# Kernel tuning notes

Hardware: AMD Instinct MI355X
Metric: run time of the kernel (lower is better)

## Reference

```python
import jax, jax.numpy as jnp
import numpy as np

C0 = 16          # embed channels (c0) == mamba d_model
OUT_DIM = 32
D_INNER = 32     # expand * c0
D_STATE = 16
D_CONV = 4
DT_RANK = 1      # max(1, d_model // 16)
EPS = 1e-5


def setup_inputs():
    key = jax.random.key(0)
    ks = jax.random.split(key, 32)

    def n(i, shape, s):
        return (jax.random.normal(ks[i], shape) * s).astype(jnp.float32)

    inp = {
        "x": jax.random.normal(ks[0], (1, 4, 64, 64, 64), jnp.float32),
        "embed_w": n(1, (4, C0, 1, 7, 7, 7), 0.1),   # 4 per-modality conv7 stems
        "ln_g": jnp.ones((C0,), jnp.float32),
        "ln_b": jnp.zeros((C0,), jnp.float32),
        "in_proj_w": n(2, (2 * D_INNER, C0), 0.25),
        "out_proj_w": n(3, (C0, D_INNER), 0.18),
        "up_w": n(4, (C0, OUT_DIM, 2, 2, 2), 0.2),   # ConvTranspose3d k=2 s=2
    }
    for j, sfx in enumerate(["", "_b"]):             # forward / backward scan params
        b = 5 + 7 * j
        inp["conv_w" + sfx] = n(b, (D_INNER, 1, D_CONV), 0.3)
        inp["conv_b" + sfx] = n(b + 1, (D_INNER,), 0.1)
        inp["xproj_w" + sfx] = n(b + 2, (DT_RANK + 2 * D_STATE, D_INNER), 0.15)
        inp["dtproj_w" + sfx] = n(b + 3, (D_INNER, DT_RANK), 0.5)
        inp["dtproj_b" + sfx] = jnp.full((D_INNER,), -4.6, jnp.float32)  # softplus ~= 0.01
        inp["A_log" + sfx] = jnp.log(jnp.tile(jnp.arange(1, D_STATE + 1, dtype=jnp.float32), (D_INNER, 1)))
        inp["D_skip" + sfx] = jnp.ones((D_INNER,), jnp.float32)
    return inp


def _instnorm(x):
    m = jnp.mean(x, axis=(2, 3, 4), keepdims=True)
    v = jnp.mean(jnp.square(x - m), axis=(2, 3, 4), keepdims=True)
    return (x - m) / jnp.sqrt(v + EPS)


def _embed(x1, w):
    # Conv3d(1, c0, k=7, s=2, p=3, bias=False) -> InstanceNorm3d -> GELU(exact)
    y = jax.lax.conv_general_dilated(x1, w, (2, 2, 2), [(3, 3)] * 3,
                                     dimension_numbers=('NCDHW', 'OIDHW', 'NCDHW'))
    return jax.nn.gelu(_instnorm(y), approximate=False)


def _branch(u, z, cw, cb, xw, dtw, dtb, A_log, D_skip):
    # One Mamba scan branch. u, z: [B, L, Dn]
    Dn = u.shape[-1]
    uc = jax.lax.conv_general_dilated(jnp.swapaxes(u, 1, 2), cw, (1,), [(D_CONV - 1, 0)],
                                      feature_group_count=Dn,
                                      dimension_numbers=('NCH', 'OIH', 'NCH'))
    u = jax.nn.silu(jnp.swapaxes(uc + cb[None, :, None], 1, 2))       # causal dw-conv + SiLU
    xdbl = u @ xw.T                                                   # [B,L,R+2N]
    dt = jax.nn.softplus(xdbl[..., :DT_RANK] @ dtw.T + dtb)           # [B,L,Dn]
    Bm = xdbl[..., DT_RANK:DT_RANK + D_STATE]                         # [B,L,N]
    Cm = xdbl[..., DT_RANK + D_STATE:]                                # [B,L,N]
    A = -jnp.exp(A_log)                                               # [Dn,N]
    a = jnp.exp(dt[..., None] * A)                                    # [B,L,Dn,N]
    b = (dt * u)[..., None] * Bm[:, :, None, :]                       # [B,L,Dn,N]

    def comb(c1, c2):
        a1, b1 = c1
        a2, b2 = c2
        return a1 * a2, a2 * b1 + b2

    _, h = jax.lax.associative_scan(comb, (a, b), axis=1)             # h_t = a_t h_{t-1} + b_t
    y = jnp.einsum('bldn,bln->bld', h, Cm) + u * D_skip
    return y * jax.nn.silu(z)


def _bimamba(t, p):
    xz = t @ p['in_proj_w'].T
    xi, z = jnp.split(xz, 2, axis=-1)
    yf = _branch(xi, z, p['conv_w'], p['conv_b'], p['xproj_w'], p['dtproj_w'],
                 p['dtproj_b'], p['A_log'], p['D_skip'])
    yb = _branch(xi[:, ::-1], z[:, ::-1], p['conv_w_b'], p['conv_b_b'], p['xproj_w_b'],
                 p['dtproj_w_b'], p['dtproj_b_b'], p['A_log_b'], p['D_skip_b'])[:, ::-1]
    return (yf + yb) @ p['out_proj_w'].T


def _mamba_dir(x5, p):
    B, C = x5.shape[:2]
    t = jnp.swapaxes(x5.reshape(B, C, -1), 1, 2)                      # [B, L, C]
    mu = jnp.mean(t, axis=-1, keepdims=True)
    var = jnp.mean(jnp.square(t - mu), axis=-1, keepdims=True)
    t = (t - mu) / jnp.sqrt(var + EPS) * p['ln_g'] + p['ln_b']        # LayerNorm
    t = _bimamba(t, p)
    return jnp.swapaxes(t, 1, 2).reshape(x5.shape)


def _mamba_layer(x5, p):
    # tri-directional scans: (d,w,h), (w,d,h), (h,w,d) + residual
    o1 = _mamba_dir(x5, p)
    o2 = jnp.transpose(_mamba_dir(jnp.transpose(x5, (0, 1, 3, 2, 4)), p), (0, 1, 3, 2, 4))
    o3 = jnp.transpose(_mamba_dir(jnp.transpose(x5, (0, 1, 4, 3, 2)), p), (0, 1, 4, 3, 2))
    return o1 + o2 + o3 + x5


def reference(x, embed_w, ln_g, ln_b, in_proj_w, out_proj_w, up_w,
              conv_w, conv_b, xproj_w, dtproj_w, dtproj_b, A_log, D_skip,
              conv_w_b, conv_b_b, xproj_w_b, dtproj_w_b, dtproj_b_b, A_log_b, D_skip_b):
    p = dict(ln_g=ln_g, ln_b=ln_b, in_proj_w=in_proj_w, out_proj_w=out_proj_w,
             conv_w=conv_w, conv_b=conv_b, xproj_w=xproj_w, dtproj_w=dtproj_w,
             dtproj_b=dtproj_b, A_log=A_log, D_skip=D_skip,
             conv_w_b=conv_w_b, conv_b_b=conv_b_b, xproj_w_b=xproj_w_b,
             dtproj_w_b=dtproj_w_b, dtproj_b_b=dtproj_b_b, A_log_b=A_log_b,
             D_skip_b=D_skip_b)
    us = [_embed(x[:, m:m + 1], embed_w[m]) for m in range(4)]        # 4 modalities
    outs = [_mamba_layer(u, p) for u in us]
    y = outs[0] + outs[1] + outs[2] + outs[3] + us[0] + us[1] + us[2] + us[3]
    B, _, D, H, W = y.shape
    # ConvTranspose3d(c0, out_dim, k=2, s=2): each output 2x2x2 block from one input voxel
    y = jnp.einsum('bcdhw,coijk->bodihjwk', y, up_w).reshape(B, OUT_DIM, 2 * D, 2 * H, 2 * W)
    return y
```

## Files before the change

kernel.cpp:

```cpp
#include <hip/hip_runtime.h>
#include <math.h>

#define L 32768
#define CH 64
#define NC 512

__device__ __forceinline__ int sigma_map(int l, int perm) {
    int b2 = l >> 10, b1 = (l >> 5) & 31, b0 = l & 31;
    if (perm == 0) return (b2 << 10) | (b1 << 5) | b0;
    if (perm == 1) return (b1 << 10) | (b2 << 5) | b0;
    return (b0 << 10) | (b1 << 5) | b2;
}

__device__ __forceinline__ float silu_f(float v) {
    return v / (1.f + __expf(-v));
}
__device__ __forceinline__ float softplus_f(float x) {
    return fmaxf(x, 0.f) + log1pf(__expf(-fabsf(x)));
}

__device__ __forceinline__ float row16_sum(float x) {
    int v;
    v = __builtin_amdgcn_update_dpp(0, __float_as_int(x), 0x128, 0xf, 0xf, true);
    x += __int_as_float(v);
    v = __builtin_amdgcn_update_dpp(0, __float_as_int(x), 0x124, 0xf, 0xf, true);
    x += __int_as_float(v);
    v = __builtin_amdgcn_update_dpp(0, __float_as_int(x), 0x122, 0xf, 0xf, true);
    x += __int_as_float(v);
    v = __builtin_amdgcn_update_dpp(0, __float_as_int(x), 0x121, 0xf, 0xf, true);
    x += __int_as_float(v);
    return x;
}

__global__ __launch_bounds__(256) void k_embed(const float* __restrict__ x,
                                               const float* __restrict__ w,
                                               float* __restrict__ us) {
    __shared__ float tile[10143];
    int bx = blockIdx.x, m = blockIdx.y;
    int c = bx >> 7, sb = bx & 127;
    int zc = sb >> 2, yc0 = (sb & 3) << 3;
    const float* xin = x + m * 262144;
    int iz0 = 2 * zc - 3, iy0 = 2 * yc0 - 3;
    for (int i = threadIdx.x; i < 10143; i += 256) {
        int tz = i / 1449, r = i - tz * 1449;
        int ty = r / 69, tx = r - ty * 69;
        int gz = iz0 + tz, gy = iy0 + ty, gx = tx - 3;
        float v = 0.f;
        if ((unsigned)gz < 64u && (unsigned)gy < 64u && (unsigned)gx < 64u)
            v = xin[(gz * 64 + gy) * 64 + gx];
        tile[i] = v;
    }
    __syncthreads();
    const float* wc = w + (m * 16 + c) * 343;
    int tyl = threadIdx.x >> 5, xc = threadIdx.x & 31;
    float acc = 0.f;
    for (int kz = 0; kz < 7; ++kz)
        for (int ky = 0; ky < 7; ++ky) {
            const float* row = &tile[(kz * 21 + 2 * tyl + ky) * 69 + 2 * xc];
            const float* wr = &wc[kz * 49 + ky * 7];
            #pragma unroll
            for (int kx = 0; kx < 7; ++kx) acc += row[kx] * wr[kx];
        }
    us[(m * 16 + c) * 32768 + sb * 256 + threadIdx.x] = acc;
}

__global__ void k_instnorm_gelu(float* __restrict__ us) {
    int ch = blockIdx.x;
    float* p = us + ch * 32768;
    float s = 0.f, s2 = 0.f;
    for (int i = threadIdx.x; i < 32768; i += 256) { float v = p[i]; s += v; s2 += v * v; }
    __shared__ float rs[256], rs2[256];
    rs[threadIdx.x] = s; rs2[threadIdx.x] = s2;
    __syncthreads();
    for (int o = 128; o > 0; o >>= 1) {
        if (threadIdx.x < o) { rs[threadIdx.x] += rs[threadIdx.x + o]; rs2[threadIdx.x] += rs2[threadIdx.x + o]; }
        __syncthreads();
    }
    float mu = rs[0] * (1.f / 32768.f);
    float var = rs2[0] * (1.f / 32768.f) - mu * mu;
    float rinv = rsqrtf(var + 1e-5f);
    for (int i = threadIdx.x; i < 32768; i += 256) {
        float v = (p[i] - mu) * rinv;
        p[i] = 0.5f * v * (1.f + erff(v * 0.70710678118654752f));
    }
}

__global__ void k_transpose(const float* __restrict__ us, float* __restrict__ us_t) {
    __shared__ float tl[16][257];
    int m = blockIdx.x >> 7, t0 = (blockIdx.x & 127) << 8;
    for (int i = threadIdx.x; i < 4096; i += 256) {
        int c = i >> 8, j = i & 255;
        tl[c][j] = us[(m * 16 + c) * 32768 + t0 + j];
    }
    __syncthreads();
    for (int i = threadIdx.x; i < 4096; i += 256) {
        int j = i >> 4, c = i & 15;
        us_t[(m * 32768 + t0 + j) * 16 + c] = tl[c][j];
    }
}

__global__ __launch_bounds__(512) void k_chunkA(
    const float* __restrict__ us_t, const float* __restrict__ ln_g, const float* __restrict__ ln_b,
    const float* __restrict__ Wip,
    const float* __restrict__ cwA, const float* __restrict__ cbA, const float* __restrict__ xwA,
    const float* __restrict__ dtwA, const float* __restrict__ dtbA, const float* __restrict__ AlA,
    const float* __restrict__ cwB, const float* __restrict__ cbB, const float* __restrict__ xwB,
    const float* __restrict__ dtwB, const float* __restrict__ dtbB, const float* __restrict__ AlB,
    float2* __restrict__ hlPa) {
    __shared__ float sm[7808];
    float* xiT = sm;
    float* uSh = sm + 2304;
    float* sB  = sm + 4480;
    float* xd0 = sm + 5568;
    float* G   = sm + 5632;

    int c = blockIdx.x, dir = blockIdx.y;
    int m = dir / 3, perm = dir - m * 3;
    int p0 = c * CH;
    int tid = threadIdx.x;

    G[tid] = Wip[tid];
    if (tid < 16) G[512 + tid] = ln_g[tid];
    else if (tid < 32) G[512 + tid] = ln_b[tid - 16];
    __syncthreads();

    if (tid < 70) {
        int p = p0 - 3 + tid;
        if ((unsigned)p < (unsigned)L) {
            int sp = sigma_map(p, perm);
            const float4* rw = (const float4*)(us_t + (m * 32768 + sp) * 16);
            float t[16];
            ((float4*)t)[0] = rw[0]; ((float4*)t)[1] = rw[1];
            ((float4*)t)[2] = rw[2]; ((float4*)t)[3] = rw[3];
            float mu = 0.f;
            #pragma unroll
            for (int ci = 0; ci < 16; ++ci) mu += t[ci];
            mu *= (1.f / 16.f);
            float var = 0.f;
            #pragma unroll
            for (int ci = 0; ci < 16; ++ci) { float d = t[ci] - mu; var += d * d; }
            var *= (1.f / 16.f);
            float rinv = rsqrtf(var + 1e-5f);
            #pragma unroll
            for (int ci = 0; ci < 16; ++ci)
                uSh[ci * 72 + tid] = (t[ci] - mu) * rinv * G[512 + ci] + G[528 + ci];
        } else {
            #pragma unroll
            for (int ci = 0; ci < 16; ++ci) uSh[ci * 72 + tid] = 0.f;
        }
    }
    __syncthreads();

    for (int it = tid; it < 576; it += 512) {
        int d = it / 18, q = it - d * 18;
        float ax = 0.f, ay = 0.f, az = 0.f, aw = 0.f;
        #pragma unroll
        for (int ci = 0; ci < 16; ++ci) {
            float4 tq = *(const float4*)&uSh[ci * 72 + 4 * q];
            float wv = G[d * 16 + ci];
            ax += tq.x * wv; ay += tq.y * wv; az += tq.z * wv; aw += tq.w * wv;
        }
        float4 o4 = {ax, ay, az, aw};
        *(float4*)&xiT[d * 72 + 4 * q] = o4;
    }
    __syncthreads();

    for (int b = 0; b < 2; ++b) {
        const float* cw  = b ? cwB  : cwA;
        const float* cb  = b ? cbB  : cbA;
        const float* xw  = b ? xwB  : xwA;
        const float* dtw = b ? dtwB : dtwA;
        const float* dtb = b ? dtbB : dtbA;
        const float* Al  = b ? AlB  : AlA;
        for (int i = tid; i < 544; i += 512) G[i] = xw[i];
        if (tid < 128) G[544 + tid] = cw[tid];
        else if (tid < 160) G[544 + tid] = cb[tid - 128];
        __syncthreads();

        {
            int d = tid >> 4, q = tid & 15, s0 = 4 * q;
            float xr[7];
            if (b == 0) {
                #pragma unroll
                for (int j = 0; j < 7; ++j) xr[j] = xiT[d * 72 + s0 + j];
            } else {
                #pragma unroll
                for (int j = 0; j < 7; ++j) xr[j] = xiT[d * 72 + 63 - s0 + j];
            }
            float w0 = G[544 + d * 4], w1 = G[545 + d * 4], w2 = G[546 + d * 4], w3 = G[547 + d * 4];
            float bias = G[672 + d];
            #pragma unroll
            for (int i = 0; i < 4; ++i) {
                float a;
                if (b == 0) a = bias + xr[i] * w0 + xr[i + 1] * w1 + xr[i + 2] * w2 + xr[i + 3] * w3;
                else        a = bias + xr[6 - i] * w0 + xr[5 - i] * w1 + xr[4 - i] * w2 + xr[3 - i] * w3;
                uSh[d * 68 + s0 + i] = silu_f(a);
            }
        }
        __syncthreads();

        for (int it = tid; it < 272; it += 512) {
            int j = it >> 4, q = it & 15, s0 = 4 * q;
            float ax = 0.f, ay = 0.f, az = 0.f, aw = 0.f;
            #pragma unroll
            for (int ci = 0; ci < 32; ++ci) {
                float4 uq = *(const float4*)&uSh[ci * 68 + s0];
                float wv = G[j * 32 + ci];
                ax += uq.x * wv; ay += uq.y * wv; az += uq.z * wv; aw += uq.w * wv;
            }
            float4 o4 = {ax, ay, az, aw};
            if (j == 0) *(float4*)&xd0[s0] = o4;
            else        *(float4*)&sB[(j - 1) * 68 + s0] = o4;
        }
        __syncthreads();

        for (int i = tid; i < 2048; i += 512) {
            int d2 = i >> 6, s = i & 63;
            G[d2 * 68 + s] = softplus_f(xd0[s] * dtw[d2] + dtb[d2]);
        }
        __syncthreads();

        {
            int d = tid >> 4, n = tid & 15;
            float A = -__expf(Al[tid]);
            float h = 0.f, sumdt = 0.f;
            const float* dtp = &G[d * 68];
            const float* up  = &uSh[d * 68];
            const float* Bp  = &sB[n * 68];
            for (int s0 = 0; s0 < CH; s0 += 4) {
                float4 dt4 = *(const float4*)&dtp[s0];
                float4 u4  = *(const float4*)&up[s0];
                float4 B4  = *(const float4*)&Bp[s0];
                h = fmaf(__expf(dt4.x * A), h, dt4.x * u4.x * B4.x);
                h = fmaf(__expf(dt4.y * A), h, dt4.y * u4.y * B4.y);
                h = fmaf(__expf(dt4.z * A), h, dt4.z * u4.z * B4.z);
                h = fmaf(__expf(dt4.w * A), h, dt4.w * u4.w * B4.w);
                sumdt += (dt4.x + dt4.y) + (dt4.z + dt4.w);
            }
            int chunk = b ? (NC - 1 - c) : c;
            float2 v; v.x = h; v.y = __expf(sumdt * A);
            hlPa[(((size_t)(dir * 2 + b) * NC + chunk) * 512) + tid] = v;
        }
        __syncthreads();
    }
}

__global__ __launch_bounds__(512) void k_scanB(float2* __restrict__ hlPa) {
    int db = blockIdx.x;
    int t = threadIdx.x;
    float2* base = hlPa + (size_t)db * NC * 512 + t;
    float H = 0.f;
    for (int c0 = 0; c0 < NC; c0 += 8) {
        float2 v[8];
        #pragma unroll
        for (int j = 0; j < 8; ++j) v[j] = base[(c0 + j) * 512];
        #pragma unroll
        for (int j = 0; j < 8; ++j) {
            *((float*)(base + (c0 + j) * 512)) = H;
            H = fmaf(v[j].y, H, v[j].x);
        }
    }
}

__global__ __launch_bounds__(512) void k_chunkC(
    const float* __restrict__ us_t, const float* __restrict__ ln_g, const float* __restrict__ ln_b,
    const float* __restrict__ Wip, const float* __restrict__ Wout,
    const float* __restrict__ cwA, const float* __restrict__ cbA, const float* __restrict__ xwA,
    const float* __restrict__ dtwA, const float* __restrict__ dtbA, const float* __restrict__ AlA,
    const float* __restrict__ DsA,
    const float* __restrict__ cwB, const float* __restrict__ cbB, const float* __restrict__ xwB,
    const float* __restrict__ dtwB, const float* __restrict__ dtbB, const float* __restrict__ AlB,
    const float* __restrict__ DsB,
    const float2* __restrict__ hlPa, float* __restrict__ O) {
    __shared__ float sm[13376];
    float* xiT = sm;
    float* zT  = sm + 2304;
    float* syT = sm + 4608;
    float* uSh = sm + 6784;
    float* sB  = sm + 8960;
    float* sC  = sm + 10048;
    float* xd0 = sm + 11136;
    float* G   = sm + 11200;

    int c = blockIdx.x, dir = blockIdx.y;
    int m = dir / 3, perm = dir - m * 3;
    int p0 = c * CH;
    int tid = threadIdx.x;

    for (int i = tid; i < 1024; i += 512) G[i] = Wip[i];
    if (tid < 16) G[1024 + tid] = ln_g[tid];
    else if (tid < 32) G[1024 + tid] = ln_b[tid - 16];
    __syncthreads();

    if (tid < 70) {
        int p = p0 - 3 + tid;
        if ((unsigned)p < (unsigned)L) {
            int sp = sigma_map(p, perm);
            const float4* rw = (const float4*)(us_t + (m * 32768 + sp) * 16);
            float t[16];
            ((float4*)t)[0] = rw[0]; ((float4*)t)[1] = rw[1];
            ((float4*)t)[2] = rw[2]; ((float4*)t)[3] = rw[3];
            float mu = 0.f;
            #pragma unroll
            for (int ci = 0; ci < 16; ++ci) mu += t[ci];
            mu *= (1.f / 16.f);
            float var = 0.f;
            #pragma unroll
            for (int ci = 0; ci < 16; ++ci) { float d = t[ci] - mu; var += d * d; }
            var *= (1.f / 16.f);
            float rinv = rsqrtf(var + 1e-5f);
            #pragma unroll
            for (int ci = 0; ci < 16; ++ci)
                uSh[ci * 72 + tid] = (t[ci] - mu) * rinv * G[1024 + ci] + G[1040 + ci];
        } else {
            #pragma unroll
            for (int ci = 0; ci < 16; ++ci) uSh[ci * 72 + tid] = 0.f;
        }
    }
    __syncthreads();

    for (int it = tid; it < 1152; it += 512) {
        int dd = it / 18, q = it - dd * 18;
        float ax = 0.f, ay = 0.f, az = 0.f, aw = 0.f;
        #pragma unroll
        for (int ci = 0; ci < 16; ++ci) {
            float4 tq = *(const float4*)&uSh[ci * 72 + 4 * q];
            float wv = G[dd * 16 + ci];
            ax += tq.x * wv; ay += tq.y * wv; az += tq.z * wv; aw += tq.w * wv;
        }
        float4 o4 = {ax, ay, az, aw};
        int d = dd & 31;
        if (dd < 32) *(float4*)&xiT[d * 72 + 4 * q] = o4;
        else         *(float4*)&zT[d * 72 + 4 * q] = o4;
    }
    __syncthreads();

    for (int b = 0; b < 2; ++b) {
        const float* cw  = b ? cwB  : cwA;
        const float* cb  = b ? cbB  : cbA;
        const float* xw  = b ? xwB  : xwA;
        const float* dtw = b ? dtwB : dtwA;
        const float* dtb = b ? dtbB : dtbA;
        const float* Al  = b ? AlB  : AlA;
        const float* Ds  = b ? DsB  : DsA;
        for (int i = tid; i < 1056; i += 512) G[i] = xw[i];
        if (tid < 128) G[1056 + tid] = cw[tid];
        else if (tid < 160) G[1056 + tid] = cb[tid - 128];
        __syncthreads();

        {
            int d = tid >> 4, q = tid & 15, s0 = 4 * q;
            float xr[7];
            if (b == 0) {
                #pragma unroll
                for (int j = 0; j < 7; ++j) xr[j] = xiT[d * 72 + s0 + j];
            } else {
                #pragma unroll
                for (int j = 0; j < 7; ++j) xr[j] = xiT[d * 72 + 63 - s0 + j];
            }
            float w0 = G[1056 + d * 4], w1 = G[1057 + d * 4], w2 = G[1058 + d * 4], w3 = G[1059 + d * 4];
            float bias = G[1184 + d];
            #pragma unroll
            for (int i = 0; i < 4; ++i) {
                float a;
                if (b == 0) a = bias + xr[i] * w0 + xr[i + 1] * w1 + xr[i + 2] * w2 + xr[i + 3] * w3;
                else        a = bias + xr[6 - i] * w0 + xr[5 - i] * w1 + xr[4 - i] * w2 + xr[3 - i] * w3;
                uSh[d * 68 + s0 + i] = silu_f(a);
            }
        }
        __syncthreads();

        for (int it = tid; it < 528; it += 512) {
            int j = it >> 4, q = it & 15, s0 = 4 * q;
            float ax = 0.f, ay = 0.f, az = 0.f, aw = 0.f;
            #pragma unroll
            for (int ci = 0; ci < 32; ++ci) {
                float4 uq = *(const float4*)&uSh[ci * 68 + s0];
                float wv = G[j * 32 + ci];
                ax += uq.x * wv; ay += uq.y * wv; az += uq.z * wv; aw += uq.w * wv;
            }
            float4 o4 = {ax, ay, az, aw};
            if (j == 0)      *(float4*)&xd0[s0] = o4;
            else if (j < 17) *(float4*)&sB[(j - 1) * 68 + s0] = o4;
            else             *(float4*)&sC[(j - 17) * 68 + s0] = o4;
        }
        __syncthreads();

        for (int i = tid; i < 2048; i += 512) {
            int d2 = i >> 6, s = i & 63;
            G[d2 * 68 + s] = softplus_f(xd0[s] * dtw[d2] + dtb[d2]);
        }
        __syncthreads();

        {
            int d = tid >> 4, n = tid & 15;
            float A = -__expf(Al[tid]);
            int chunk = b ? (NC - 1 - c) : c;
            float h = hlPa[(((size_t)(dir * 2 + b) * NC + chunk) * 512) + tid].x;
            const float* dtp = &G[d * 68];
            const float* up  = &uSh[d * 68];
            const float* Bp  = &sB[n * 68];
            const float* Cp  = &sC[n * 68];
            for (int s0 = 0; s0 < CH; s0 += 4) {
                float4 dt4 = *(const float4*)&dtp[s0];
                float4 u4  = *(const float4*)&up[s0];
                float4 B4  = *(const float4*)&Bp[s0];
                float4 C4  = *(const float4*)&Cp[s0];
                float pr0, pr1, pr2, pr3;
                h = fmaf(__expf(dt4.x * A), h, dt4.x * u4.x * B4.x); pr0 = row16_sum(h * C4.x);
                h = fmaf(__expf(dt4.y * A), h, dt4.y * u4.y * B4.y); pr1 = row16_sum(h * C4.y);
                h = fmaf(__expf(dt4.z * A), h, dt4.z * u4.z * B4.z); pr2 = row16_sum(h * C4.z);
                h = fmaf(__expf(dt4.w * A), h, dt4.w * u4.w * B4.w); pr3 = row16_sum(h * C4.w);
                if (n == 0) {
                    if (b == 0) {
                        float4 o4 = {pr0, pr1, pr2, pr3};
                        *(float4*)&syT[d * 68 + s0] = o4;
                    } else {
                        float4* dst = (float4*)&syT[d * 68 + (60 - s0)];
                        float4 old = *dst;
                        old.x += pr3; old.y += pr2; old.z += pr1; old.w += pr0;
                        *dst = old;
                    }
                }
            }
        }
        __syncthreads();

        for (int it = tid; it < 2048; it += 512) {
            int d = it >> 6, s = it & 63;
            int pl = b ? (63 - s) : s;
            syT[d * 68 + pl] += uSh[d * 68 + s] * Ds[d];
        }
        __syncthreads();
    }

    for (int it = tid; it < 2048; it += 512) {
        int d = it >> 6, pl = it & 63;
        syT[d * 68 + pl] *= silu_f(zT[d * 72 + pl + 3]);
    }
    __syncthreads();

    if (tid < 512) G[tid] = Wout[tid];
    __syncthreads();
    for (int it = tid; it < 1024; it += 512) {
        int p = it >> 4, cc = it & 15;
        float acc = 0.f;
        #pragma unroll
        for (int d = 0; d < 32; ++d) acc += syT[d * 68 + p] * G[cc * 32 + d];
        O[((size_t)(dir * 32768 + p0 + p)) * 16 + cc] = acc;
    }
}

__global__ void k_accum(const float* __restrict__ us_t, const float* __restrict__ O,
                        float* __restrict__ acc_t) {
    int it = blockIdx.x * 256 + threadIdx.x;
    int sp = it >> 2, q = (it & 3) << 2;
    float ax = 0.f, ay = 0.f, az = 0.f, aw = 0.f;
    #pragma unroll
    for (int mm = 0; mm < 4; ++mm) {
        float4 v = *(const float4*)&us_t[(mm * 32768 + sp) * 16 + q];
        ax += 2.f * v.x; ay += 2.f * v.y; az += 2.f * v.z; aw += 2.f * v.w;
    }
    #pragma unroll
    for (int perm = 0; perm < 3; ++perm) {
        int l = sigma_map(sp, perm);
        #pragma unroll
        for (int mm = 0; mm < 4; ++mm) {
            int dir = mm * 3 + perm;
            float4 v = *(const float4*)&O[(dir * 32768 + l) * 16 + q];
            ax += v.x; ay += v.y; az += v.z; aw += v.w;
        }
    }
    float4 o4 = {ax, ay, az, aw};
    *(float4*)&acc_t[sp * 16 + q] = o4;
}

__global__ void k_up(const float* __restrict__ acc_t, const float* __restrict__ upw,
                     float* __restrict__ out) {
    __shared__ float w[4096];
    for (int i = threadIdx.x; i < 4096; i += 256) w[i] = upw[i];
    __syncthreads();
    int e = blockIdx.x * 256 + threadIdx.x;
    int o = e >> 17;
    int r2 = e & 131071;
    int Dz = r2 >> 11, Hy = (r2 >> 5) & 63, Wp = r2 & 31;
    int sp = ((Dz >> 1) << 10) | ((Hy >> 1) << 5) | Wp;
    int wbase = (((Dz & 1) << 2) | ((Hy & 1) << 1));
    const float* arow = &acc_t[sp * 16];
    float v0 = 0.f, v1 = 0.f;
    #pragma unroll
    for (int c = 0; c < 16; ++c) {
        float a = arow[c];
        const float* wr = &w[(c * 32 + o) * 8 + wbase];
        v0 += a * wr[0];
        v1 += a * wr[1];
    }
    float2 ov; ov.x = v0; ov.y = v1;
    *(float2*)&out[((o * 64 + Dz) * 64 + Hy) * 64 + 2 * Wp] = ov;
}

extern "C" void kernel_launch(void* const* d_in, const int* in_sizes, int n_in,
                              void* d_out, int out_size, void* d_ws, size_t ws_size,
                              hipStream_t stream) {
    (void)in_sizes; (void)n_in; (void)out_size; (void)ws_size;
    const float* x    = (const float*)d_in[0];
    const float* embw = (const float*)d_in[1];
    const float* ln_g = (const float*)d_in[2];
    const float* ln_b = (const float*)d_in[3];
    const float* Wip  = (const float*)d_in[4];
    const float* Wout = (const float*)d_in[5];
    const float* upw  = (const float*)d_in[6];
    const float* cwA  = (const float*)d_in[7];
    const float* cbA  = (const float*)d_in[8];
    const float* xwA  = (const float*)d_in[9];
    const float* dtwA = (const float*)d_in[10];
    const float* dtbA = (const float*)d_in[11];
    const float* AlA  = (const float*)d_in[12];
    const float* DsA  = (const float*)d_in[13];
    const float* cwB  = (const float*)d_in[14];
    const float* cbB  = (const float*)d_in[15];
    const float* xwB  = (const float*)d_in[16];
    const float* dtwB = (const float*)d_in[17];
    const float* dtbB = (const float*)d_in[18];
    const float* AlB  = (const float*)d_in[19];
    const float* DsB  = (const float*)d_in[20];

    float* ws    = (float*)d_ws;
    float*  us    = ws;
    float*  us_t  = ws + 2097152;
    float2* hlPa  = (float2*)(ws + 4194304);
    float*  O     = ws + 16777216;
    float*  acc_t = ws + 23068672;

    k_embed<<<dim3(2048, 4), 256, 0, stream>>>(x, embw, us);
    k_instnorm_gelu<<<64, 256, 0, stream>>>(us);
    k_transpose<<<512, 256, 0, stream>>>(us, us_t);
    k_chunkA<<<dim3(NC, 12), 512, 0, stream>>>(us_t, ln_g, ln_b, Wip,
                                               cwA, cbA, xwA, dtwA, dtbA, AlA,
                                               cwB, cbB, xwB, dtwB, dtbB, AlB, hlPa);
    k_scanB<<<24, 512, 0, stream>>>(hlPa);
    k_chunkC<<<dim3(NC, 12), 512, 0, stream>>>(us_t, ln_g, ln_b, Wip, Wout,
                                               cwA, cbA, xwA, dtwA, dtbA, AlA, DsA,
                                               cwB, cbB, xwB, dtwB, dtbB, AlB, DsB,
                                               hlPa, O);
    k_accum<<<512, 256, 0, stream>>>(us_t, O, acc_t);
    k_up<<<16384, 256, 0, stream>>>(acc_t, upw, (float*)d_out);
}
```

Before: 857.4 us.

## Give each scan thread four states, transpose B/C layout, use exp2

The selective scan in both chunk kernels now has each thread hold four state values (128 threads instead of 512). B and C are stored time-major so one float4 load serves four states. The C-reduction shrinks from a 16-lane DPP row sum to a local FMA plus a 2-step quad sum, and the exponentials become a native exp2 with the log2(e) factor folded in. The D-skip term is now written before the scan. Fewer threads run the serial recurrence, which lowers parallelism per block in exchange for fewer shuffles and less redundant loading of dt and u.

```diff
diff --git a/kernel.cpp b/kernel.cpp
--- a/kernel.cpp
+++ b/kernel.cpp
@@ -4,6 +4,12 @@
 #define L 32768
 #define CH 64
 #define NC 512
+
+#if __has_builtin(__builtin_amdgcn_exp2f)
+#define EXP2(x) __builtin_amdgcn_exp2f(x)
+#else
+#define EXP2(x) exp2f(x)
+#endif
 
 __device__ __forceinline__ int sigma_map(int l, int perm) {
     int b2 = l >> 10, b1 = (l >> 5) & 31, b0 = l & 31;
@@ -19,15 +25,10 @@
     return fmaxf(x, 0.f) + log1pf(__expf(-fabsf(x)));
 }
 
-__device__ __forceinline__ float row16_sum(float x) {
-    int v;
-    v = __builtin_amdgcn_update_dpp(0, __float_as_int(x), 0x128, 0xf, 0xf, true);
+__device__ __forceinline__ float quad_sum(float x) {
+    int v = __builtin_amdgcn_update_dpp(0, __float_as_int(x), 0xB1, 0xf, 0xf, true);
     x += __int_as_float(v);
-    v = __builtin_amdgcn_update_dpp(0, __float_as_int(x), 0x124, 0xf, 0xf, true);
-    x += __int_as_float(v);
-    v = __builtin_amdgcn_update_dpp(0, __float_as_int(x), 0x122, 0xf, 0xf, true);
-    x += __int_as_float(v);
-    v = __builtin_amdgcn_update_dpp(0, __float_as_int(x), 0x121, 0xf, 0xf, true);
+    v = __builtin_amdgcn_update_dpp(0, __float_as_int(x), 0x4E, 0xf, 0xf, true);
     x += __int_as_float(v);
     return x;
 }
@@ -107,12 +108,12 @@
     const float* __restrict__ cwB, const float* __restrict__ cbB, const float* __restrict__ xwB,
     const float* __restrict__ dtwB, const float* __restrict__ dtbB, const float* __restrict__ AlB,
     float2* __restrict__ hlPa) {
-    __shared__ float sm[7808];
+    __shared__ float sm[8000];
     float* xiT = sm;
     float* uSh = sm + 2304;
-    float* sB  = sm + 4480;
-    float* xd0 = sm + 5568;
-    float* G   = sm + 5632;
+    float* sBs = sm + 4480;
+    float* xd0 = sm + 5760;
+    float* G   = sm + 5824;
 
     int c = blockIdx.x, dir = blockIdx.y;
     int m = dir / 3, perm = dir - m * 3;
@@ -208,9 +209,15 @@
                 float wv = G[j * 32 + ci];
                 ax += uq.x * wv; ay += uq.y * wv; az += uq.z * wv; aw += uq.w * wv;
             }
-            float4 o4 = {ax, ay, az, aw};
-            if (j == 0) *(float4*)&xd0[s0] = o4;
-            else        *(float4*)&sB[(j - 1) * 68 + s0] = o4;
+            if (j == 0) {
+                float4 o4 = {ax, ay, az, aw};
+                *(float4*)&xd0[s0] = o4;
+            } else {
+                sBs[(s0 + 0) * 20 + (j - 1)] = ax;
+                sBs[(s0 + 1) * 20 + (j - 1)] = ay;
+                sBs[(s0 + 2) * 20 + (j - 1)] = az;
+                sBs[(s0 + 3) * 20 + (j - 1)] = aw;
+            }
         }
         __syncthreads();
 
@@ -220,26 +227,37 @@
         }
         __syncthreads();
 
-        {
-            int d = tid >> 4, n = tid & 15;
-            float A = -__expf(Al[tid]);
-            float h = 0.f, sumdt = 0.f;
+        if (tid < 128) {
+            int d = tid >> 2, nb = (tid & 3) * 4;
+            float kk0 = -1.44269504f * __expf(Al[d * 16 + nb + 0]);
+            float kk1 = -1.44269504f * __expf(Al[d * 16 + nb + 1]);
+            float kk2 = -1.44269504f * __expf(Al[d * 16 + nb + 2]);
+            float kk3 = -1.44269504f * __expf(Al[d * 16 + nb + 3]);
+            float h0 = 0.f, h1 = 0.f, h2 = 0.f, h3 = 0.f, sumdt = 0.f;
             const float* dtp = &G[d * 68];
             const float* up  = &uSh[d * 68];
-            const float* Bp  = &sB[n * 68];
             for (int s0 = 0; s0 < CH; s0 += 4) {
                 float4 dt4 = *(const float4*)&dtp[s0];
                 float4 u4  = *(const float4*)&up[s0];
-                float4 B4  = *(const float4*)&Bp[s0];
-                h = fmaf(__expf(dt4.x * A), h, dt4.x * u4.x * B4.x);
-                h = fmaf(__expf(dt4.y * A), h, dt4.y * u4.y * B4.y);
-                h = fmaf(__expf(dt4.z * A), h, dt4.z * u4.z * B4.z);
-                h = fmaf(__expf(dt4.w * A), h, dt4.w * u4.w * B4.w);
-                sumdt += (dt4.x + dt4.y) + (dt4.z + dt4.w);
+                #define ASTEP(DT, UU, SS) { \
+                    float w_ = (DT) * (UU); \
+                    float4 B4 = *(const float4*)&sBs[(SS) * 20 + nb]; \
+                    h0 = fmaf(EXP2((DT) * kk0), h0, w_ * B4.x); \
+                    h1 = fmaf(EXP2((DT) * kk1), h1, w_ * B4.y); \
+                    h2 = fmaf(EXP2((DT) * kk2), h2, w_ * B4.z); \
+                    h3 = fmaf(EXP2((DT) * kk3), h3, w_ * B4.w); \
+                    sumdt += (DT); }
+                ASTEP(dt4.x, u4.x, s0 + 0)
+                ASTEP(dt4.y, u4.y, s0 + 1)
+                ASTEP(dt4.z, u4.z, s0 + 2)
+                ASTEP(dt4.w, u4.w, s0 + 3)
+                #undef ASTEP
             }
             int chunk = b ? (NC - 1 - c) : c;
-            float2 v; v.x = h; v.y = __expf(sumdt * A);
-            hlPa[(((size_t)(dir * 2 + b) * NC + chunk) * 512) + tid] = v;
+            float4* o4 = (float4*)(hlPa + (((size_t)(dir * 2 + b) * NC + chunk) * 512) + d * 16 + nb);
+            float4 a0 = {h0, EXP2(sumdt * kk0), h1, EXP2(sumdt * kk1)};
+            float4 a1 = {h2, EXP2(sumdt * kk2), h3, EXP2(sumdt * kk3)};
+            o4[0] = a0; o4[1] = a1;
         }
         __syncthreads();
     }
@@ -272,15 +290,15 @@
     const float* __restrict__ dtwB, const float* __restrict__ dtbB, const float* __restrict__ AlB,
     const float* __restrict__ DsB,
     const float2* __restrict__ hlPa, float* __restrict__ O) {
-    __shared__ float sm[13376];
+    __shared__ float sm[13504];
     float* xiT = sm;
     float* zT  = sm + 2304;
     float* syT = sm + 4608;
     float* uSh = sm + 6784;
-    float* sB  = sm + 8960;
-    float* sC  = sm + 10048;
-    float* xd0 = sm + 11136;
-    float* G   = sm + 11200;
+    float* sBs = sm + 8960;
+    float* sCs = sm + 10240;
+    float* xd0 = sm + 11264;
+    float* G   = sm + 11328;
 
     int c = blockIdx.x, dir = blockIdx.y;
     int m = dir / 3, perm = dir - m * 3;
@@ -379,10 +397,20 @@
                 float wv = G[j * 32 + ci];
                 ax += uq.x * wv; ay += uq.y * wv; az += uq.z * wv; aw += uq.w * wv;
             }
-            float4 o4 = {ax, ay, az, aw};
-            if (j == 0)      *(float4*)&xd0[s0] = o4;
-            else if (j < 17) *(float4*)&sB[(j - 1) * 68 + s0] = o4;
-            else             *(float4*)&sC[(j - 17) * 68 + s0] = o4;
+            if (j == 0) {
+                float4 o4 = {ax, ay, az, aw};
+                *(float4*)&xd0[s0] = o4;
+            } else if (j < 17) {
+                sBs[(s0 + 0) * 20 + (j - 1)] = ax;
+                sBs[(s0 + 1) * 20 + (j - 1)] = ay;
+                sBs[(s0 + 2) * 20 + (j - 1)] = az;
+                sBs[(s0 + 3) * 20 + (j - 1)] = aw;
+            } else {
+                sCs[(s0 + 0) * 16 + (j - 17)] = ax;
+                sCs[(s0 + 1) * 16 + (j - 17)] = ay;
+                sCs[(s0 + 2) * 16 + (j - 17)] = az;
+                sCs[(s0 + 3) * 16 + (j - 17)] = aw;
+            }
         }
         __syncthreads();
 
@@ -392,44 +420,61 @@
         }
         __syncthreads();
 
-        {
-            int d = tid >> 4, n = tid & 15;
-            float A = -__expf(Al[tid]);
+        for (int it = tid; it < 2048; it += 512) {
+            int d = it >> 6, s = it & 63;
+            float val = uSh[d * 68 + s] * Ds[d];
+            if (b == 0) syT[d * 68 + s] = val;
+            else        syT[d * 68 + (63 - s)] += val;
+        }
+        __syncthreads();
+
+        if (tid < 128) {
+            int d = tid >> 2, nb = (tid & 3) * 4;
+            float kk0 = -1.44269504f * __expf(Al[d * 16 + nb + 0]);
+            float kk1 = -1.44269504f * __expf(Al[d * 16 + nb + 1]);
+            float kk2 = -1.44269504f * __expf(Al[d * 16 + nb + 2]);
+            float kk3 = -1.44269504f * __expf(Al[d * 16 + nb + 3]);
             int chunk = b ? (NC - 1 - c) : c;
-            float h = hlPa[(((size_t)(dir * 2 + b) * NC + chunk) * 512) + tid].x;
+            const float2* hp = hlPa + (((size_t)(dir * 2 + b) * NC + chunk) * 512) + d * 16 + nb;
+            float h0 = hp[0].x, h1 = hp[1].x, h2 = hp[2].x, h3 = hp[3].x;
             const float* dtp = &G[d * 68];
             const float* up  = &uSh[d * 68];
-            const float* Bp  = &sB[n * 68];
-            const float* Cp  = &sC[n * 68];
             for (int s0 = 0; s0 < CH; s0 += 4) {
                 float4 dt4 = *(const float4*)&dtp[s0];
                 float4 u4  = *(const float4*)&up[s0];
-                float4 B4  = *(const float4*)&Bp[s0];
-                float4 C4  = *(const float4*)&Cp[s0];
                 float pr0, pr1, pr2, pr3;
-                h = fmaf(__expf(dt4.x * A), h, dt4.x * u4.x * B4.x); pr0 = row16_sum(h * C4.x);
-                h = fmaf(__expf(dt4.y * A), h, dt4.y * u4.y * B4.y); pr1 = row16_sum(h * C4.y);
-                h = fmaf(__expf(dt4.z * A), h, dt4.z * u4.z * B4.z); pr2 = row16_sum(h * C4.z);
-                h = fmaf(__expf(dt4.w * A), h, dt4.w * u4.w * B4.w); pr3 = row16_sum(h * C4.w);
-                if (n == 0) {
+                #define CSTEP(DT, UU, SS, PR) { \
+                    float w_ = (DT) * (UU); \
+                    float4 B4 = *(const float4*)&sBs[(SS) * 20 + nb]; \
+                    float4 C4 = *(const float4*)&sCs[(SS) * 16 + nb]; \
+                    h0 = fmaf(EXP2((DT) * kk0), h0, w_ * B4.x); \
+                    h1 = fmaf(EXP2((DT) * kk1), h1, w_ * B4.y); \
+                    h2 = fmaf(EXP2((DT) * kk2), h2, w_ * B4.z); \
+                    h3 = fmaf(EXP2((DT) * kk3), h3, w_ * B4.w); \
+                    float p_ = h0 * C4.x; \
+                    p_ = fmaf(h1, C4.y, p_); \
+                    p_ = fmaf(h2, C4.z, p_); \
+                    p_ = fmaf(h3, C4.w, p_); \
+                    PR = quad_sum(p_); }
+                CSTEP(dt4.x, u4.x, s0 + 0, pr0)
+                CSTEP(dt4.y, u4.y, s0 + 1, pr1)
+                CSTEP(dt4.z, u4.z, s0 + 2, pr2)
+                CSTEP(dt4.w, u4.w, s0 + 3, pr3)
+                #undef CSTEP
+                if ((tid & 3) == 0) {
                     if (b == 0) {
-                        float4 o4 = {pr0, pr1, pr2, pr3};
-                        *(float4*)&syT[d * 68 + s0] = o4;
+                        float4* dst = (float4*)&syT[d * 68 + s0];
+                        float4 o = *dst;
+                        o.x += pr0; o.y += pr1; o.z += pr2; o.w += pr3;
+                        *dst = o;
                     } else {
                         float4* dst = (float4*)&syT[d * 68 + (60 - s0)];
-                        float4 old = *dst;
-                        old.x += pr3; old.y += pr2; old.z += pr1; old.w += pr0;
-                        *dst = old;
+                        float4 o = *dst;
+                        o.x += pr3; o.y += pr2; o.z += pr1; o.w += pr0;
+                        *dst = o;
                     }
                 }
             }
-        }
-        __syncthreads();
-
-        for (int it = tid; it < 2048; it += 512) {
-            int d = it >> 6, s = it & 63;
-            int pl = b ? (63 - s) : s;
-            syT[d * 68 + pl] += uSh[d * 68 + s] * Ds[d];
         }
         __syncthreads();
     }
```

Measured after the change: 928.7 us. 8.3% more time.
